# Performance work log

Measured on AMD Instinct MI355X. Metric: run time of the kernel, lower is better.

The kernel has to match this reference:

```python
import jax, jax.numpy as jnp
import numpy as np

B, N, D, H, DH, E, BIAS_DIM = 8, 512, 512, 8, 64, 32768, 8

def setup_inputs() -> dict:
    key = jax.random.key(0)
    ks = jax.random.split(key, 10)
    states = jax.random.normal(ks[0], (B, N, D), jnp.float32)
    key_states = jax.random.normal(ks[1], (B, N, D), jnp.float32)
    # causal mask, broadcastable over heads: [B,1,N,N]
    masks = jnp.broadcast_to(jnp.tril(jnp.ones((N, N), jnp.float32)), (B, 1, N, N))
    edge_type = jax.random.randint(ks[2], (E, 1), 0, BIAS_DIM, jnp.int32)
    b_idx = jax.random.randint(ks[3], (E, 1), 0, B, jnp.int32)
    q_idx = jax.random.randint(ks[4], (E, 1), 0, N, jnp.int32)
    k_idx = jax.random.randint(ks[5], (E, 1), 0, N, jnp.int32)
    attention_bias = jnp.concatenate([edge_type, b_idx, q_idx, k_idx], axis=1)
    s = 0.05
    Wq = jax.random.normal(ks[6], (D, H, DH), jnp.float32) * s
    Wk = jax.random.normal(ks[7], (D, H, DH), jnp.float32) * s
    Wv = jax.random.normal(ks[8], (D, H, DH), jnp.float32) * s
    k2 = jax.random.split(ks[9], 3)
    Wo = jax.random.normal(k2[0], (H, DH, D), jnp.float32) * s
    bias_embs = jax.random.normal(k2[1], (BIAS_DIM, DH), jnp.float32) * s
    bias_scalar = jax.random.normal(k2[2], (DH, 1), jnp.float32) * s
    return {"states": states, "key_states": key_states, "masks": masks,
            "attention_bias": attention_bias, "Wq": Wq, "Wk": Wk, "Wv": Wv,
            "Wo": Wo, "bias_embs": bias_embs, "bias_scalar": bias_scalar}

def reference(states, key_states, masks, attention_bias, Wq, Wk, Wv, Wo, bias_embs, bias_scalar):
    q = jnp.einsum('btd,dha->btha', states, Wq)
    k = jnp.einsum('btd,dha->btha', key_states, Wk)
    v = jnp.einsum('btd,dha->btha', key_states, Wv)
    alpha = jnp.einsum('bkha,bqha->bhqk', k, q)  # [B,H,Q,K]
    # sparse edge bias: embed edge types, project to scalar, scatter into [B,Q,K]
    et = attention_bias[:, 0]
    bias_vals = (bias_embs[et] @ bias_scalar)[:, 0]  # [E]
    bq, bk = alpha.shape[2], alpha.shape[3]
    bias_mat = jnp.zeros((alpha.shape[0], bq, bk), alpha.dtype)
    bias_mat = bias_mat.at[attention_bias[:, 1], attention_bias[:, 2], attention_bias[:, 3]].add(bias_vals)
    summed_keys = jnp.sum(k, axis=-1)  # [B,K,H]
    alpha = alpha + jnp.einsum('bqk,bkh->bhqk', bias_mat, summed_keys)
    alpha = alpha * jax.lax.rsqrt(jnp.float32(DH))
    neg = jnp.finfo(jnp.float32).min
    alpha = alpha * masks + (1.0 - jnp.ceil(masks)) * neg
    alpha = jax.nn.softmax(alpha, axis=-1)
    alpha = alpha * masks
    context = jnp.einsum('bhqk,bkha->bqha', alpha, v)
    return jnp.einsum('btha,had->btd', context, Wo)
```

## Files before the change

kernel.cpp:

```cpp
#include <hip/hip_runtime.h>

typedef unsigned short u16;
typedef unsigned int u32;
typedef __bf16 bf16x8 __attribute__((ext_vector_type(8)));
typedef float f32x4 __attribute__((ext_vector_type(4)));
typedef u16 u16x8 __attribute__((ext_vector_type(8)));
typedef u16 u16x4 __attribute__((ext_vector_type(4)));


__device__ __forceinline__ u16 f2b(float f) {
  union { float f; u32 i; } v; v.f = f;
  u32 r = v.i + 0x7fffu + ((v.i >> 16) & 1u);
  return (u16)(r >> 16);
}
__device__ __forceinline__ float b2f(u16 u) {
  union { u32 i; float f; } v; v.i = ((u32)u) << 16; return v.f;
}
__device__ __forceinline__ u16x8 pack8(float4 x0, float4 x1) {
  u16x8 p;
  p[0] = f2b(x0.x); p[1] = f2b(x0.y); p[2] = f2b(x0.z); p[3] = f2b(x0.w);
  p[4] = f2b(x1.x); p[5] = f2b(x1.y); p[6] = f2b(x1.z); p[7] = f2b(x1.w);
  return p;
}

__global__ __launch_bounds__(256) void prologue(
    const float* __restrict__ Wq, const float* __restrict__ Wk,
    const float* __restrict__ Wv, const float* __restrict__ Wo,
    const int* __restrict__ ab, const float* __restrict__ be,
    const float* __restrict__ bsc,
    u16* __restrict__ wbase, float* __restrict__ bias_mat, int n_edges) {
  __shared__ u16 t[32][33];
  __shared__ float tv[8];
  int bid = blockIdx.x;
  int tid = threadIdx.x;
  if (bid < 1024) {
    int z = bid >> 8, rem = bid & 255;
    int bx = rem & 15, by = rem >> 4;
    const float* src; float sc = 1.f;
    if (z == 0)      { src = Wq; sc = 0.125f; }
    else if (z == 1) { src = Wk; }
    else if (z == 2) { src = Wv; }
    else             { src = Wo; }
    u16* dst = wbase + (size_t)z * 262144;
    int tx = tid & 31, ty = tid >> 5;
    int c0 = bx * 32, r0 = by * 32;
    #pragma unroll
    for (int i = ty; i < 32; i += 8) t[i][tx] = f2b(src[(r0 + i) * 512 + c0 + tx] * sc);
    __syncthreads();
    #pragma unroll
    for (int i = ty; i < 32; i += 8) dst[(c0 + i) * 512 + r0 + tx] = t[tx][i];
  } else {
    if (tid < 8) {
      float s = 0.f;
      #pragma unroll
      for (int a = 0; a < 64; a++) s += be[tid * 64 + a] * bsc[a];
      tv[tid] = s * 0.125f;
    }
    __syncthreads();
    int e = (bid - 1024) * 256 + tid;
    if (e < n_edges) {
      int et = ab[e * 4 + 0];
      int b  = ab[e * 4 + 1];
      int qi = ab[e * 4 + 2];
      int ki = ab[e * 4 + 3];
      atomicAdd(&bias_mat[((size_t)b * 512 + qi) * 512 + ki], tv[et]);
    }
  }
}

__global__ __launch_bounds__(256) void qkv_gemm(const float* __restrict__ states,
                                                const float* __restrict__ key_states,
                                                const u16* __restrict__ wT,
                                                u16* __restrict__ qb,
                                                u16* __restrict__ kbo,
                                                u16* __restrict__ vtb,
                                                float* __restrict__ summed) {
  __shared__ u16 As[64 * 72];
  __shared__ u16 Bs[128 * 72];
  __shared__ float ssum[4][64];
  int tid = threadIdx.x;
  int lane = tid & 63, wave = tid >> 6;
  int quad = lane >> 4, ln = lane & 15;
  int row0 = blockIdx.x * 64;
  int col0 = blockIdx.y * 128;
  const float* A = (col0 < 512) ? states : key_states;
  int ara = tid >> 2, aca = (tid & 3) * 16;
  int arb = tid >> 1, acb = (tid & 1) * 32;

  f32x4 acc[4][2];
  #pragma unroll
  for (int i = 0; i < 4; i++)
    #pragma unroll
    for (int j = 0; j < 2; j++) acc[i][j] = (f32x4){0.f, 0.f, 0.f, 0.f};

  const float* ap = A + (size_t)(row0 + ara) * 512 + aca;
  const u16* bp = wT + (size_t)(col0 + arb) * 512 + acb;

  float4 fa0, fa1, fa2, fa3;
  u16x8 rb0, rb1, rb2, rb3;
  fa0 = ((const float4*)ap)[0]; fa1 = ((const float4*)ap)[1];
  fa2 = ((const float4*)ap)[2]; fa3 = ((const float4*)ap)[3];
  rb0 = *(const u16x8*)(bp + 0);  rb1 = *(const u16x8*)(bp + 8);
  rb2 = *(const u16x8*)(bp + 16); rb3 = *(const u16x8*)(bp + 24);

  for (int k0 = 0; k0 < 512; k0 += 64) {
    u16x8 pa0 = pack8(fa0, fa1);
    u16x8 pa1 = pack8(fa2, fa3);
    __syncthreads();
    *(u16x8*)&As[ara * 72 + aca + 0] = pa0;  *(u16x8*)&As[ara * 72 + aca + 8] = pa1;
    *(u16x8*)&Bs[arb * 72 + acb + 0]  = rb0;  *(u16x8*)&Bs[arb * 72 + acb + 8]  = rb1;
    *(u16x8*)&Bs[arb * 72 + acb + 16] = rb2;  *(u16x8*)&Bs[arb * 72 + acb + 24] = rb3;
    __syncthreads();
    if (k0 < 448) {
      int kn = k0 + 64;
      const float4* apn = (const float4*)(ap + kn);
      fa0 = apn[0]; fa1 = apn[1]; fa2 = apn[2]; fa3 = apn[3];
      rb0 = *(const u16x8*)(bp + kn + 0);  rb1 = *(const u16x8*)(bp + kn + 8);
      rb2 = *(const u16x8*)(bp + kn + 16); rb3 = *(const u16x8*)(bp + kn + 24);
    }
    #pragma unroll
    for (int s = 0; s < 2; s++) {
      bf16x8 af[4], bfv[2];
      #pragma unroll
      for (int i = 0; i < 4; i++)
        af[i] = *(bf16x8*)&As[(i * 16 + ln) * 72 + s * 32 + quad * 8];
      #pragma unroll
      for (int j = 0; j < 2; j++)
        bfv[j] = *(bf16x8*)&Bs[(wave * 32 + j * 16 + ln) * 72 + s * 32 + quad * 8];
      #pragma unroll
      for (int i = 0; i < 4; i++)
        #pragma unroll
        for (int j = 0; j < 2; j++)
          acc[i][j] = __builtin_amdgcn_mfma_f32_16x16x32_bf16(af[i], bfv[j], acc[i][j], 0, 0, 0);
    }
  }

  int region = col0 >> 9;
  int nbase = col0 & 511;
  if (region <= 1) {
    u16* Cout = region ? kbo : qb;
    #pragma unroll
    for (int i = 0; i < 4; i++)
      #pragma unroll
      for (int j = 0; j < 2; j++) {
        int mb = row0 + i * 16 + quad * 4;
        int n = nbase + wave * 32 + j * 16 + ln;
        #pragma unroll
        for (int r = 0; r < 4; r++)
          Cout[(size_t)(mb + r) * 512 + n] = f2b(acc[i][j][r]);
      }
    if (region == 1) {
      #pragma unroll
      for (int i = 0; i < 4; i++)
        #pragma unroll
        for (int r = 0; r < 4; r++) {
          float v = acc[i][0][r] + acc[i][1][r];
          v += __shfl_xor(v, 1);
          v += __shfl_xor(v, 2);
          v += __shfl_xor(v, 4);
          v += __shfl_xor(v, 8);
          if (ln == 0) ssum[wave][i * 16 + quad * 4 + r] = v;
        }
      __syncthreads();
      if (tid < 128) {
        int hl = tid >> 6, row = tid & 63;
        float s = ssum[hl * 2][row] + ssum[hl * 2 + 1][row];
        int m = row0 + row;
        int b = m >> 9, t = m & 511;
        int h = (nbase >> 6) + hl;
        summed[((size_t)(b * 8 + h)) * 512 + t] = s;
      }
    }
  } else {
    #pragma unroll
    for (int i = 0; i < 4; i++)
      #pragma unroll
      for (int j = 0; j < 2; j++) {
        int mb = row0 + i * 16 + quad * 4;
        int bb = mb >> 9, t0 = mb & 511;
        int a_abs = nbase + wave * 32 + j * 16 + ln;
        int h = a_abs >> 6, a = a_abs & 63;
        u16x4 p;
        p[0] = f2b(acc[i][j][0]); p[1] = f2b(acc[i][j][1]);
        p[2] = f2b(acc[i][j][2]); p[3] = f2b(acc[i][j][3]);
        *(u16x4*)&vtb[(((size_t)bb * 8 + h) * 64 + a) * 512 + t0] = p;
      }
  }
}

__global__ __launch_bounds__(256) void out_gemm(const u16* __restrict__ A,
                                                const u16* __restrict__ BT,
                                                float* __restrict__ C) {
  __shared__ u16 As[64 * 72];
  __shared__ u16 Bs[64 * 72];
  int tid = threadIdx.x;
  int lane = tid & 63, wave = tid >> 6;
  int quad = lane >> 4, ln = lane & 15;
  int wr = wave >> 1, wc = wave & 1;
  int row0 = blockIdx.x * 64;
  int col0 = blockIdx.y * 64;
  int ar = tid >> 2, ac = (tid & 3) * 16;

  f32x4 acc[2][2];
  #pragma unroll
  for (int i = 0; i < 2; i++)
    #pragma unroll
    for (int j = 0; j < 2; j++) acc[i][j] = (f32x4){0.f, 0.f, 0.f, 0.f};

  const u16* ap = A + (size_t)(row0 + ar) * 512 + ac;
  const u16* bp = BT + (size_t)(col0 + ar) * 512 + ac;

  u16x8 ra0, ra1, rb0, rb1;
  ra0 = *(const u16x8*)(ap + 0); ra1 = *(const u16x8*)(ap + 8);
  rb0 = *(const u16x8*)(bp + 0); rb1 = *(const u16x8*)(bp + 8);

  for (int k0 = 0; k0 < 512; k0 += 64) {
    __syncthreads();
    *(u16x8*)&As[ar * 72 + ac + 0] = ra0;  *(u16x8*)&As[ar * 72 + ac + 8] = ra1;
    *(u16x8*)&Bs[ar * 72 + ac + 0] = rb0;  *(u16x8*)&Bs[ar * 72 + ac + 8] = rb1;
    __syncthreads();
    if (k0 < 448) {
      int kn = k0 + 64;
      ra0 = *(const u16x8*)(ap + kn + 0); ra1 = *(const u16x8*)(ap + kn + 8);
      rb0 = *(const u16x8*)(bp + kn + 0); rb1 = *(const u16x8*)(bp + kn + 8);
    }
    #pragma unroll
    for (int s = 0; s < 2; s++) {
      bf16x8 af[2], bfv[2];
      #pragma unroll
      for (int i = 0; i < 2; i++)
        af[i] = *(bf16x8*)&As[(wr * 32 + i * 16 + ln) * 72 + s * 32 + quad * 8];
      #pragma unroll
      for (int j = 0; j < 2; j++)
        bfv[j] = *(bf16x8*)&Bs[(wc * 32 + j * 16 + ln) * 72 + s * 32 + quad * 8];
      #pragma unroll
      for (int i = 0; i < 2; i++)
        #pragma unroll
        for (int j = 0; j < 2; j++)
          acc[i][j] = __builtin_amdgcn_mfma_f32_16x16x32_bf16(af[i], bfv[j], acc[i][j], 0, 0, 0);
    }
  }
  #pragma unroll
  for (int i = 0; i < 2; i++)
    #pragma unroll
    for (int j = 0; j < 2; j++) {
      int mb = row0 + wr * 32 + i * 16 + quad * 4;
      int n = col0 + wc * 32 + j * 16 + ln;
      #pragma unroll
      for (int r = 0; r < 4; r++)
        C[(size_t)(mb + r) * 512 + n] = acc[i][j][r];
    }
}

__global__ __launch_bounds__(256) void attn_mfma(const u16* __restrict__ q,
                                                 const u16* __restrict__ k,
                                                 const u16* __restrict__ vt,
                                                 const float* __restrict__ bias_mat,
                                                 const float* __restrict__ summed,
                                                 u16* __restrict__ ctx,
                                                 float* __restrict__ Opart,
                                                 float* __restrict__ ml) {
  __shared__ u16 Qs[64 * 72];
  __shared__ u16 Ks[64 * 72];
  __shared__ u16 Vt[64 * 72];
  __shared__ u16 Ps[4][16 * 72];
  int tid = threadIdx.x;
  int wave = tid >> 6, lane = tid & 63;
  int quad = lane >> 4, ln = lane & 15;
  int p2 = blockIdx.x;
  int bh, u;
  {
    const int fours[6] = {3, 4, 6, 8, 10, 11};
    const int threes[2] = {2, 9};
    const int ones[2] = {0, 5};
    const int twos[2] = {1, 7};
    if (p2 < 384)      { bh = p2 & 63; u = fours[p2 >> 6]; }
    else if (p2 < 512) { int q2 = p2 - 384; bh = q2 & 63; u = threes[q2 >> 6]; }
    else if (p2 < 640) { int q2 = p2 - 512; bh = q2 & 63; u = ones[q2 >> 6]; }
    else               { int q2 = p2 - 640; bh = q2 & 63; u = twos[q2 >> 6]; }
  }
  int b = bh >> 3, h = bh & 7;
  int qt, kb0, kbe, part = 0;
  bool partial;
  if (u < 4) { qt = u; kb0 = 0; kbe = u; partial = false; }
  else {
    int v = u - 4; qt = 4 + (v >> 1); part = v & 1; partial = true;
    if (part == 0) { kb0 = 0; kbe = 3; } else { kb0 = 4; kbe = qt; }
  }
  int q0 = qt * 64;

  int sr = tid >> 2;
  int sc2 = (tid & 3) * 16;

  {
    const u16* qp = q + ((size_t)(b * 512 + q0 + sr)) * 512 + h * 64 + sc2;
    *(u16x8*)&Qs[sr * 72 + sc2] = *(const u16x8*)qp;
    *(u16x8*)&Qs[sr * 72 + sc2 + 8] = *(const u16x8*)(qp + 8);
  }

  float m_r[4], l_r[4];
  f32x4 o[4];
  #pragma unroll
  for (int r = 0; r < 4; r++) { m_r[r] = -3.40282347e38f; l_r[r] = 0.f; }
  #pragma unroll
  for (int nt = 0; nt < 4; nt++) o[nt] = (f32x4){0.f, 0.f, 0.f, 0.f};

  const u16* kp0 = k + ((size_t)(b * 512 + sr)) * 512 + h * 64 + sc2;
  const u16* vp0 = vt + ((size_t)(bh * 64 + sr)) * 512 + sc2;

  u16x8 rk0 = *(const u16x8*)(kp0 + (size_t)kb0 * 64 * 512);
  u16x8 rk1 = *(const u16x8*)(kp0 + (size_t)kb0 * 64 * 512 + 8);
  u16x8 rv0 = *(const u16x8*)(vp0 + kb0 * 64);
  u16x8 rv1 = *(const u16x8*)(vp0 + kb0 * 64 + 8);

  int qrow = q0 + wave * 16 + quad * 4;

  float c_skv[4], c_bias[4][4];
  #pragma unroll
  for (int nt = 0; nt < 4; nt++) {
    int t = kb0 * 64 + nt * 16 + ln;
    c_skv[nt] = summed[bh * 512 + t];
    const float* bp2 = bias_mat + ((size_t)(b * 512 + qrow)) * 512 + t;
    #pragma unroll
    for (int r = 0; r < 4; r++) c_bias[nt][r] = bp2[(size_t)r * 512];
  }

  for (int kb = kb0; kb <= kbe; kb++) {
    __syncthreads();
    *(u16x8*)&Ks[sr * 72 + sc2] = rk0;
    *(u16x8*)&Ks[sr * 72 + sc2 + 8] = rk1;
    *(u16x8*)&Vt[sr * 72 + sc2] = rv0;
    *(u16x8*)&Vt[sr * 72 + sc2 + 8] = rv1;
    __syncthreads();

    float n_skv[4], n_bias[4][4];
    if (kb < kbe) {
      const u16* kp = kp0 + (size_t)(kb + 1) * 64 * 512;
      const u16* vp = vp0 + (kb + 1) * 64;
      rk0 = *(const u16x8*)kp;
      rk1 = *(const u16x8*)(kp + 8);
      rv0 = *(const u16x8*)vp;
      rv1 = *(const u16x8*)(vp + 8);
      #pragma unroll
      for (int nt = 0; nt < 4; nt++) {
        int t = (kb + 1) * 64 + nt * 16 + ln;
        n_skv[nt] = summed[bh * 512 + t];
        const float* bp2 = bias_mat + ((size_t)(b * 512 + qrow)) * 512 + t;
        #pragma unroll
        for (int r = 0; r < 4; r++) n_bias[nt][r] = bp2[(size_t)r * 512];
      }
    }

    bf16x8 aq0 = *(bf16x8*)&Qs[(wave * 16 + ln) * 72 + quad * 8];
    bf16x8 aq1 = *(bf16x8*)&Qs[(wave * 16 + ln) * 72 + 32 + quad * 8];
    f32x4 s[4];
    #pragma unroll
    for (int nt = 0; nt < 4; nt++) {
      bf16x8 b0 = *(bf16x8*)&Ks[(nt * 16 + ln) * 72 + quad * 8];
      bf16x8 b1 = *(bf16x8*)&Ks[(nt * 16 + ln) * 72 + 32 + quad * 8];
      s[nt] = (f32x4){0.f, 0.f, 0.f, 0.f};
      s[nt] = __builtin_amdgcn_mfma_f32_16x16x32_bf16(aq0, b0, s[nt], 0, 0, 0);
      s[nt] = __builtin_amdgcn_mfma_f32_16x16x32_bf16(aq1, b1, s[nt], 0, 0, 0);
    }

    #pragma unroll
    for (int nt = 0; nt < 4; nt++) {
      int t = kb * 64 + nt * 16 + ln;
      #pragma unroll
      for (int r = 0; r < 4; r++) {
        float val = s[nt][r] + c_bias[nt][r] * c_skv[nt];
        s[nt][r] = (t <= qrow + r) ? val : -3.40282347e38f;
      }
    }

    float alpha[4];
    #pragma unroll
    for (int r = 0; r < 4; r++) {
      float tm = fmaxf(fmaxf(s[0][r], s[1][r]), fmaxf(s[2][r], s[3][r]));
      #pragma unroll
      for (int off = 8; off; off >>= 1) tm = fmaxf(tm, __shfl_xor(tm, off));
      float mn = fmaxf(m_r[r], tm);
      alpha[r] = __expf(m_r[r] - mn);
      m_r[r] = mn;
      float rs = 0.f;
      #pragma unroll
      for (int nt = 0; nt < 4; nt++) {
        float pp = __expf(s[nt][r] - mn);
        s[nt][r] = pp;
        rs += pp;
      }
      #pragma unroll
      for (int off = 8; off; off >>= 1) rs += __shfl_xor(rs, off);
      l_r[r] = l_r[r] * alpha[r] + rs;
    }

    #pragma unroll
    for (int nt = 0; nt < 4; nt++)
      #pragma unroll
      for (int r = 0; r < 4; r++)
        Ps[wave][(quad * 4 + r) * 72 + nt * 16 + ln] = f2b(s[nt][r]);
    #pragma unroll
    for (int nt = 0; nt < 4; nt++)
      #pragma unroll
      for (int r = 0; r < 4; r++)
        o[nt][r] *= alpha[r];

    bf16x8 ap0 = *(bf16x8*)&Ps[wave][ln * 72 + quad * 8];
    bf16x8 ap1 = *(bf16x8*)&Ps[wave][ln * 72 + 32 + quad * 8];
    #pragma unroll
    for (int nt = 0; nt < 4; nt++) {
      bf16x8 b0 = *(bf16x8*)&Vt[(nt * 16 + ln) * 72 + quad * 8];
      bf16x8 b1 = *(bf16x8*)&Vt[(nt * 16 + ln) * 72 + 32 + quad * 8];
      o[nt] = __builtin_amdgcn_mfma_f32_16x16x32_bf16(ap0, b0, o[nt], 0, 0, 0);
      o[nt] = __builtin_amdgcn_mfma_f32_16x16x32_bf16(ap1, b1, o[nt], 0, 0, 0);
    }

    if (kb < kbe) {
      #pragma unroll
      for (int nt = 0; nt < 4; nt++) {
        c_skv[nt] = n_skv[nt];
        #pragma unroll
        for (int r = 0; r < 4; r++) c_bias[nt][r] = n_bias[nt][r];
      }
    }
  }

  if (!partial) {
    #pragma unroll
    for (int r = 0; r < 4; r++) {
      float inv = 1.f / l_r[r];
      int qr2 = qrow + r;
      u16* dst = ctx + ((size_t)(b * 512 + qr2)) * 512 + h * 64;
      #pragma unroll
      for (int nt = 0; nt < 4; nt++)
        dst[nt * 16 + ln] = f2b(o[nt][r] * inv);
    }
  } else {
    #pragma unroll
    for (int r = 0; r < 4; r++) {
      int row = qrow + r - 256;
      float* dst = Opart + (((size_t)(part * 64 + bh)) * 256 + row) * 64;
      #pragma unroll
      for (int nt = 0; nt < 4; nt++)
        dst[nt * 16 + ln] = o[nt][r];
    }
    if (ln == 0) {
      #pragma unroll
      for (int r = 0; r < 4; r++) {
        int row = qrow + r - 256;
        float* mp = ml + (((size_t)(part * 64 + bh)) * 256 + row) * 2;
        mp[0] = m_r[r];
        mp[1] = l_r[r];
      }
    }
  }
}

__global__ __launch_bounds__(256) void attn_merge(const float* __restrict__ Opart,
                                                  const float* __restrict__ ml,
                                                  u16* __restrict__ ctx) {
  int gid = blockIdx.x * 256 + threadIdx.x;
  int col = gid & 63;
  int row = (gid >> 6) & 255;
  int bh = gid >> 14;
  size_t i0 = (size_t)bh * 256 + row;
  size_t i1 = (size_t)(64 + bh) * 256 + row;
  float m0 = ml[i0 * 2], l0 = ml[i0 * 2 + 1];
  float m1 = ml[i1 * 2], l1 = ml[i1 * 2 + 1];
  float m = fmaxf(m0, m1);
  float a0 = __expf(m0 - m), a1 = __expf(m1 - m);
  float l = l0 * a0 + l1 * a1;
  float O0 = Opart[i0 * 64 + col], O1 = Opart[i1 * 64 + col];
  float val = (O0 * a0 + O1 * a1) / l;
  int b = bh >> 3, h = bh & 7, qrow = 256 + row;
  ctx[((size_t)(b * 512 + qrow)) * 512 + h * 64 + col] = f2b(val);
}

extern "C" void kernel_launch(void* const* d_in, const int* in_sizes, int n_in,
                              void* d_out, int out_size, void* d_ws, size_t ws_size,
                              hipStream_t stream) {
  const float* states     = (const float*)d_in[0];
  const float* key_states = (const float*)d_in[1];
  const int*   ab         = (const int*)d_in[3];
  const float* Wq         = (const float*)d_in[4];
  const float* Wk         = (const float*)d_in[5];
  const float* Wv         = (const float*)d_in[6];
  const float* Wo         = (const float*)d_in[7];
  const float* be         = (const float*)d_in[8];
  const float* bsc        = (const float*)d_in[9];
  float* out = (float*)d_out;

  char* ws = (char*)d_ws;
  const size_t MB = 1024 * 1024;
  u16* wbase    = (u16*)(ws);
  u16* wot      = (u16*)(ws + 1536 * 1024);
  u16* qb       = (u16*)(ws + 2 * MB);
  u16* kbo      = (u16*)(ws + 6 * MB);
  u16* vtb      = (u16*)(ws + 10 * MB);
  u16* ctxb     = (u16*)(ws + 14 * MB);
  float* bias_m = (float*)(ws + 18 * MB);
  float* summed = (float*)(ws + 26 * MB);
  float* Opart  = (float*)(ws + 27 * MB);
  float* mlbuf  = (float*)(ws + 35 * MB);

  int n_edges = in_sizes[3] / 4;

  hipMemsetAsync(bias_m, 0, (size_t)8 * MB, stream);
  prologue<<<dim3(1024 + (n_edges + 255) / 256), 256, 0, stream>>>(
      Wq, Wk, Wv, Wo, ab, be, bsc, wbase, bias_m, n_edges);
  qkv_gemm<<<dim3(64, 12), 256, 0, stream>>>(states, key_states, wbase, qb, kbo, vtb, summed);
  attn_mfma<<<dim3(768), 256, 0, stream>>>(qb, kbo, vtb, bias_m, summed, ctxb, Opart, mlbuf);
  attn_merge<<<dim3(4096), 256, 0, stream>>>(Opart, mlbuf, ctxb);
  out_gemm<<<dim3(64, 8), 256, 0, stream>>>(ctxb, wot, out);
}
```

Measured before the change: 135.4 us.

## Fuse split-KV merge into output GEMM and fold memset and scatter into existing kernels

Removes the hipMemset and the separate attn_merge launch. The prologue now zeroes the bias matrix alongside the weight transposes. The edge-bias atomic scatter moves into extra blocks of the QKV GEMM launch, and the output GEMM combines the two partial attention outputs on the fly for the second half of query rows. This cuts two launches and a round trip of the merged context through global memory. In exchange, the out_gemm A-tile load path for merged rows reads twice the fp32 data and does exp and normalization work per tile.

```diff
diff --git a/kernel.cpp b/kernel.cpp
--- a/kernel.cpp
+++ b/kernel.cpp
@@ -13,9 +13,6 @@
   u32 r = v.i + 0x7fffu + ((v.i >> 16) & 1u);
   return (u16)(r >> 16);
 }
-__device__ __forceinline__ float b2f(u16 u) {
-  union { u32 i; float f; } v; v.i = ((u32)u) << 16; return v.f;
-}
 __device__ __forceinline__ u16x8 pack8(float4 x0, float4 x1) {
   u16x8 p;
   p[0] = f2b(x0.x); p[1] = f2b(x0.y); p[2] = f2b(x0.z); p[3] = f2b(x0.w);
@@ -26,11 +23,8 @@
 __global__ __launch_bounds__(256) void prologue(
     const float* __restrict__ Wq, const float* __restrict__ Wk,
     const float* __restrict__ Wv, const float* __restrict__ Wo,
-    const int* __restrict__ ab, const float* __restrict__ be,
-    const float* __restrict__ bsc,
-    u16* __restrict__ wbase, float* __restrict__ bias_mat, int n_edges) {
+    u16* __restrict__ wbase, float* __restrict__ bias_mat) {
   __shared__ u16 t[32][33];
-  __shared__ float tv[8];
   int bid = blockIdx.x;
   int tid = threadIdx.x;
   if (bid < 1024) {
@@ -50,6 +44,33 @@
     #pragma unroll
     for (int i = ty; i < 32; i += 8) dst[(c0 + i) * 512 + r0 + tx] = t[tx][i];
   } else {
+    int gid = (bid - 1024) * 256 + tid;
+    float4 z4 = (float4){0.f, 0.f, 0.f, 0.f};
+    float4* dst = (float4*)bias_mat + (size_t)gid * 4;
+    dst[0] = z4; dst[1] = z4; dst[2] = z4; dst[3] = z4;
+  }
+}
+
+__global__ __launch_bounds__(256) void qkv_gemm(const float* __restrict__ states,
+                                                const float* __restrict__ key_states,
+                                                const u16* __restrict__ wT,
+                                                u16* __restrict__ qb,
+                                                u16* __restrict__ kbo,
+                                                u16* __restrict__ vtb,
+                                                float* __restrict__ summed,
+                                                const int* __restrict__ ab,
+                                                const float* __restrict__ be,
+                                                const float* __restrict__ bsc,
+                                                float* __restrict__ bias_mat,
+                                                int n_edges) {
+  __shared__ u16 As[64 * 72];
+  __shared__ u16 Bs[128 * 72];
+  __shared__ float ssum[4][64];
+  __shared__ float tv[8];
+  int bid = blockIdx.x;
+  int tid = threadIdx.x;
+
+  if (bid >= 768) {
     if (tid < 8) {
       float s = 0.f;
       #pragma unroll
@@ -57,7 +78,7 @@
       tv[tid] = s * 0.125f;
     }
     __syncthreads();
-    int e = (bid - 1024) * 256 + tid;
+    int e = (bid - 768) * 256 + tid;
     if (e < n_edges) {
       int et = ab[e * 4 + 0];
       int b  = ab[e * 4 + 1];
@@ -65,24 +86,14 @@
       int ki = ab[e * 4 + 3];
       atomicAdd(&bias_mat[((size_t)b * 512 + qi) * 512 + ki], tv[et]);
     }
-  }
-}
-
-__global__ __launch_bounds__(256) void qkv_gemm(const float* __restrict__ states,
-                                                const float* __restrict__ key_states,
-                                                const u16* __restrict__ wT,
-                                                u16* __restrict__ qb,
-                                                u16* __restrict__ kbo,
-                                                u16* __restrict__ vtb,
-                                                float* __restrict__ summed) {
-  __shared__ u16 As[64 * 72];
-  __shared__ u16 Bs[128 * 72];
-  __shared__ float ssum[4][64];
-  int tid = threadIdx.x;
+    return;
+  }
+
   int lane = tid & 63, wave = tid >> 6;
   int quad = lane >> 4, ln = lane & 15;
-  int row0 = blockIdx.x * 64;
-  int col0 = blockIdx.y * 128;
+  int bx = bid & 63, by = bid >> 6;
+  int row0 = bx * 64;
+  int col0 = by * 128;
   const float* A = (col0 < 512) ? states : key_states;
   int ara = tid >> 2, aca = (tid & 3) * 16;
   int arb = tid >> 1, acb = (tid & 1) * 32;
@@ -186,70 +197,6 @@
         *(u16x4*)&vtb[(((size_t)bb * 8 + h) * 64 + a) * 512 + t0] = p;
       }
   }
-}
-
-__global__ __launch_bounds__(256) void out_gemm(const u16* __restrict__ A,
-                                                const u16* __restrict__ BT,
-                                                float* __restrict__ C) {
-  __shared__ u16 As[64 * 72];
-  __shared__ u16 Bs[64 * 72];
-  int tid = threadIdx.x;
-  int lane = tid & 63, wave = tid >> 6;
-  int quad = lane >> 4, ln = lane & 15;
-  int wr = wave >> 1, wc = wave & 1;
-  int row0 = blockIdx.x * 64;
-  int col0 = blockIdx.y * 64;
-  int ar = tid >> 2, ac = (tid & 3) * 16;
-
-  f32x4 acc[2][2];
-  #pragma unroll
-  for (int i = 0; i < 2; i++)
-    #pragma unroll
-    for (int j = 0; j < 2; j++) acc[i][j] = (f32x4){0.f, 0.f, 0.f, 0.f};
-
-  const u16* ap = A + (size_t)(row0 + ar) * 512 + ac;
-  const u16* bp = BT + (size_t)(col0 + ar) * 512 + ac;
-
-  u16x8 ra0, ra1, rb0, rb1;
-  ra0 = *(const u16x8*)(ap + 0); ra1 = *(const u16x8*)(ap + 8);
-  rb0 = *(const u16x8*)(bp + 0); rb1 = *(const u16x8*)(bp + 8);
-
-  for (int k0 = 0; k0 < 512; k0 += 64) {
-    __syncthreads();
-    *(u16x8*)&As[ar * 72 + ac + 0] = ra0;  *(u16x8*)&As[ar * 72 + ac + 8] = ra1;
-    *(u16x8*)&Bs[ar * 72 + ac + 0] = rb0;  *(u16x8*)&Bs[ar * 72 + ac + 8] = rb1;
-    __syncthreads();
-    if (k0 < 448) {
-      int kn = k0 + 64;
-      ra0 = *(const u16x8*)(ap + kn + 0); ra1 = *(const u16x8*)(ap + kn + 8);
-      rb0 = *(const u16x8*)(bp + kn + 0); rb1 = *(const u16x8*)(bp + kn + 8);
-    }
-    #pragma unroll
-    for (int s = 0; s < 2; s++) {
-      bf16x8 af[2], bfv[2];
-      #pragma unroll
-      for (int i = 0; i < 2; i++)
-        af[i] = *(bf16x8*)&As[(wr * 32 + i * 16 + ln) * 72 + s * 32 + quad * 8];
-      #pragma unroll
-      for (int j = 0; j < 2; j++)
-        bfv[j] = *(bf16x8*)&Bs[(wc * 32 + j * 16 + ln) * 72 + s * 32 + quad * 8];
-      #pragma unroll
-      for (int i = 0; i < 2; i++)
-        #pragma unroll
-        for (int j = 0; j < 2; j++)
-          acc[i][j] = __builtin_amdgcn_mfma_f32_16x16x32_bf16(af[i], bfv[j], acc[i][j], 0, 0, 0);
-    }
-  }
-  #pragma unroll
-  for (int i = 0; i < 2; i++)
-    #pragma unroll
-    for (int j = 0; j < 2; j++) {
-      int mb = row0 + wr * 32 + i * 16 + quad * 4;
-      int n = col0 + wc * 32 + j * 16 + ln;
-      #pragma unroll
-      for (int r = 0; r < 4; r++)
-        C[(size_t)(mb + r) * 512 + n] = acc[i][j][r];
-    }
 }
 
 __global__ __launch_bounds__(256) void attn_mfma(const u16* __restrict__ q,
@@ -456,24 +403,116 @@
   }
 }
 
-__global__ __launch_bounds__(256) void attn_merge(const float* __restrict__ Opart,
-                                                  const float* __restrict__ ml,
-                                                  u16* __restrict__ ctx) {
-  int gid = blockIdx.x * 256 + threadIdx.x;
-  int col = gid & 63;
-  int row = (gid >> 6) & 255;
-  int bh = gid >> 14;
-  size_t i0 = (size_t)bh * 256 + row;
-  size_t i1 = (size_t)(64 + bh) * 256 + row;
-  float m0 = ml[i0 * 2], l0 = ml[i0 * 2 + 1];
-  float m1 = ml[i1 * 2], l1 = ml[i1 * 2 + 1];
-  float m = fmaxf(m0, m1);
-  float a0 = __expf(m0 - m), a1 = __expf(m1 - m);
-  float l = l0 * a0 + l1 * a1;
-  float O0 = Opart[i0 * 64 + col], O1 = Opart[i1 * 64 + col];
-  float val = (O0 * a0 + O1 * a1) / l;
-  int b = bh >> 3, h = bh & 7, qrow = 256 + row;
-  ctx[((size_t)(b * 512 + qrow)) * 512 + h * 64 + col] = f2b(val);
+__global__ __launch_bounds__(256) void out_gemm(const u16* __restrict__ A,
+                                                const u16* __restrict__ BT,
+                                                const float* __restrict__ Opart,
+                                                const float* __restrict__ ml,
+                                                float* __restrict__ C) {
+  __shared__ u16 As[64 * 72];
+  __shared__ u16 Bs[64 * 72];
+  int tid = threadIdx.x;
+  int lane = tid & 63, wave = tid >> 6;
+  int quad = lane >> 4, ln = lane & 15;
+  int wr = wave >> 1, wc = wave & 1;
+  int row0 = blockIdx.x * 64;
+  int col0 = blockIdx.y * 64;
+  int ar = tid >> 2, ac = (tid & 3) * 16;
+  bool merged = (row0 & 256) != 0;
+  int mrow = row0 + ar;
+  int bb = mrow >> 9;
+  int rrow = (mrow & 511) - 256;
+
+  f32x4 acc[2][2];
+  #pragma unroll
+  for (int i = 0; i < 2; i++)
+    #pragma unroll
+    for (int j = 0; j < 2; j++) acc[i][j] = (f32x4){0.f, 0.f, 0.f, 0.f};
+
+  const u16* ap = A + (size_t)mrow * 512 + ac;
+  const u16* bp = BT + (size_t)(col0 + ar) * 512 + ac;
+
+  u16x8 ra0, ra1, rb0, rb1;
+  float4 g0, g1, g2, g3, hh0, hh1, hh2, hh3;
+  float cm0, cl0, cm1, cl1;
+  if (!merged) {
+    ra0 = *(const u16x8*)(ap + 0); ra1 = *(const u16x8*)(ap + 8);
+  } else {
+    size_t i0 = (size_t)(bb * 8 + 0) * 256 + rrow;
+    size_t i1 = (size_t)(64 + bb * 8 + 0) * 256 + rrow;
+    const float4* O0 = (const float4*)(Opart + i0 * 64 + ac);
+    const float4* O1 = (const float4*)(Opart + i1 * 64 + ac);
+    g0 = O0[0]; g1 = O0[1]; g2 = O0[2]; g3 = O0[3];
+    hh0 = O1[0]; hh1 = O1[1]; hh2 = O1[2]; hh3 = O1[3];
+    cm0 = ml[i0 * 2]; cl0 = ml[i0 * 2 + 1];
+    cm1 = ml[i1 * 2]; cl1 = ml[i1 * 2 + 1];
+  }
+  rb0 = *(const u16x8*)(bp + 0); rb1 = *(const u16x8*)(bp + 8);
+
+  for (int k0 = 0; k0 < 512; k0 += 64) {
+    u16x8 pa0, pa1;
+    if (!merged) {
+      pa0 = ra0; pa1 = ra1;
+    } else {
+      float mm = fmaxf(cm0, cm1);
+      float e0 = __expf(cm0 - mm), e1 = __expf(cm1 - mm);
+      float inv = 1.f / (cl0 * e0 + cl1 * e1);
+      e0 *= inv; e1 *= inv;
+      pa0[0] = f2b(g0.x * e0 + hh0.x * e1); pa0[1] = f2b(g0.y * e0 + hh0.y * e1);
+      pa0[2] = f2b(g0.z * e0 + hh0.z * e1); pa0[3] = f2b(g0.w * e0 + hh0.w * e1);
+      pa0[4] = f2b(g1.x * e0 + hh1.x * e1); pa0[5] = f2b(g1.y * e0 + hh1.y * e1);
+      pa0[6] = f2b(g1.z * e0 + hh1.z * e1); pa0[7] = f2b(g1.w * e0 + hh1.w * e1);
+      pa1[0] = f2b(g2.x * e0 + hh2.x * e1); pa1[1] = f2b(g2.y * e0 + hh2.y * e1);
+      pa1[2] = f2b(g2.z * e0 + hh2.z * e1); pa1[3] = f2b(g2.w * e0 + hh2.w * e1);
+      pa1[4] = f2b(g3.x * e0 + hh3.x * e1); pa1[5] = f2b(g3.y * e0 + hh3.y * e1);
+      pa1[6] = f2b(g3.z * e0 + hh3.z * e1); pa1[7] = f2b(g3.w * e0 + hh3.w * e1);
+    }
+    __syncthreads();
+    *(u16x8*)&As[ar * 72 + ac + 0] = pa0;  *(u16x8*)&As[ar * 72 + ac + 8] = pa1;
+    *(u16x8*)&Bs[ar * 72 + ac + 0] = rb0;  *(u16x8*)&Bs[ar * 72 + ac + 8] = rb1;
+    __syncthreads();
+    if (k0 < 448) {
+      int kn = k0 + 64;
+      if (!merged) {
+        ra0 = *(const u16x8*)(ap + kn + 0); ra1 = *(const u16x8*)(ap + kn + 8);
+      } else {
+        int h = kn >> 6;
+        size_t i0 = (size_t)(bb * 8 + h) * 256 + rrow;
+        size_t i1 = (size_t)(64 + bb * 8 + h) * 256 + rrow;
+        const float4* O0 = (const float4*)(Opart + i0 * 64 + ac);
+        const float4* O1 = (const float4*)(Opart + i1 * 64 + ac);
+        g0 = O0[0]; g1 = O0[1]; g2 = O0[2]; g3 = O0[3];
+        hh0 = O1[0]; hh1 = O1[1]; hh2 = O1[2]; hh3 = O1[3];
+        cm0 = ml[i0 * 2]; cl0 = ml[i0 * 2 + 1];
+        cm1 = ml[i1 * 2]; cl1 = ml[i1 * 2 + 1];
+      }
+      rb0 = *(const u16x8*)(bp + kn + 0); rb1 = *(const u16x8*)(bp + kn + 8);
+    }
+    #pragma unroll
+    for (int s = 0; s < 2; s++) {
+      bf16x8 af[2], bfv[2];
+      #pragma unroll
+      for (int i = 0; i < 2; i++)
+        af[i] = *(bf16x8*)&As[(wr * 32 + i * 16 + ln) * 72 + s * 32 + quad * 8];
+      #pragma unroll
+      for (int j = 0; j < 2; j++)
+        bfv[j] = *(bf16x8*)&Bs[(wc * 32 + j * 16 + ln) * 72 + s * 32 + quad * 8];
+      #pragma unroll
+      for (int i = 0; i < 2; i++)
+        #pragma unroll
+        for (int j = 0; j < 2; j++)
+          acc[i][j] = __builtin_amdgcn_mfma_f32_16x16x32_bf16(af[i], bfv[j], acc[i][j], 0, 0, 0);
+    }
+  }
+  #pragma unroll
+  for (int i = 0; i < 2; i++)
+    #pragma unroll
+    for (int j = 0; j < 2; j++) {
+      int mb = row0 + wr * 32 + i * 16 + quad * 4;
+      int n = col0 + wc * 32 + j * 16 + ln;
+      #pragma unroll
+      for (int r = 0; r < 4; r++)
+        C[(size_t)(mb + r) * 512 + n] = acc[i][j][r];
+    }
 }
 
 extern "C" void kernel_launch(void* const* d_in, const int* in_sizes, int n_in,
@@ -505,11 +544,9 @@
 
   int n_edges = in_sizes[3] / 4;
 
-  hipMemsetAsync(bias_m, 0, (size_t)8 * MB, stream);
-  prologue<<<dim3(1024 + (n_edges + 255) / 256), 256, 0, stream>>>(
-      Wq, Wk, Wv, Wo, ab, be, bsc, wbase, bias_m, n_edges);
-  qkv_gemm<<<dim3(64, 12), 256, 0, stream>>>(states, key_states, wbase, qb, kbo, vtb, summed);
+  prologue<<<dim3(1536), 256, 0, stream>>>(Wq, Wk, Wv, Wo, wbase, bias_m);
+  qkv_gemm<<<dim3(768 + (n_edges + 255) / 256), 256, 0, stream>>>(
+      states, key_states, wbase, qb, kbo, vtb, summed, ab, be, bsc, bias_m, n_edges);
   attn_mfma<<<dim3(768), 256, 0, stream>>>(qb, kbo, vtb, bias_m, summed, ctxb, Opart, mlbuf);
-  attn_merge<<<dim3(4096), 256, 0, stream>>>(Opart, mlbuf, ctxb);
-  out_gemm<<<dim3(64, 8), 256, 0, stream>>>(ctxb, wot, out);
-}
+  out_gemm<<<dim3(64, 8), 256, 0, stream>>>(ctxb, wot, Opart, mlbuf, out);
+}
```

New measurement: 134.7 us. No clear change (-0.5%).

## Restructure attention into per-wave 16-row tiles and fold bias zeroing and scatter into other kernels

Applied to the files above, without the earlier changes.

Attention is rewritten so each wave handles one 16-row query tile. Rows are paired (j, 31-j, j+8, 23-j) so every block does a balanced amount of causal work, which removes the split-K partial path and the merge kernel. K and V fragments are loaded straight from global memory into registers, with no shared-memory staging and no block barriers. The bias matrix is now zeroed inside the prologue instead of by a memset, and the edge scatter moves into extra blocks of the QKV GEMM launch, cutting the kernel count. The trade-off is that waves no longer share K/V loads through LDS, so each wave re-reads them from global memory or cache.

```diff
diff --git a/kernel.cpp b/kernel.cpp
--- a/kernel.cpp
+++ b/kernel.cpp
@@ -13,9 +13,6 @@
   u32 r = v.i + 0x7fffu + ((v.i >> 16) & 1u);
   return (u16)(r >> 16);
 }
-__device__ __forceinline__ float b2f(u16 u) {
-  union { u32 i; float f; } v; v.i = ((u32)u) << 16; return v.f;
-}
 __device__ __forceinline__ u16x8 pack8(float4 x0, float4 x1) {
   u16x8 p;
   p[0] = f2b(x0.x); p[1] = f2b(x0.y); p[2] = f2b(x0.z); p[3] = f2b(x0.w);
@@ -26,11 +23,8 @@
 __global__ __launch_bounds__(256) void prologue(
     const float* __restrict__ Wq, const float* __restrict__ Wk,
     const float* __restrict__ Wv, const float* __restrict__ Wo,
-    const int* __restrict__ ab, const float* __restrict__ be,
-    const float* __restrict__ bsc,
-    u16* __restrict__ wbase, float* __restrict__ bias_mat, int n_edges) {
+    u16* __restrict__ wbase, float* __restrict__ bias_mat) {
   __shared__ u16 t[32][33];
-  __shared__ float tv[8];
   int bid = blockIdx.x;
   int tid = threadIdx.x;
   if (bid < 1024) {
@@ -50,6 +44,33 @@
     #pragma unroll
     for (int i = ty; i < 32; i += 8) dst[(c0 + i) * 512 + r0 + tx] = t[tx][i];
   } else {
+    int gid = (bid - 1024) * 256 + tid;
+    float4 z4 = (float4){0.f, 0.f, 0.f, 0.f};
+    float4* dst = (float4*)bias_mat + (size_t)gid * 4;
+    dst[0] = z4; dst[1] = z4; dst[2] = z4; dst[3] = z4;
+  }
+}
+
+__global__ __launch_bounds__(256) void qkv_gemm(const float* __restrict__ states,
+                                                const float* __restrict__ key_states,
+                                                const u16* __restrict__ wT,
+                                                u16* __restrict__ qb,
+                                                u16* __restrict__ kbo,
+                                                u16* __restrict__ vtb,
+                                                float* __restrict__ summed,
+                                                const int* __restrict__ ab,
+                                                const float* __restrict__ be,
+                                                const float* __restrict__ bsc,
+                                                float* __restrict__ bias_mat,
+                                                int n_edges) {
+  __shared__ u16 As[64 * 72];
+  __shared__ u16 Bs[128 * 72];
+  __shared__ float ssum[4][64];
+  __shared__ float tv[8];
+  int bid = blockIdx.x;
+  int tid = threadIdx.x;
+
+  if (bid >= 768) {
     if (tid < 8) {
       float s = 0.f;
       #pragma unroll
@@ -57,7 +78,7 @@
       tv[tid] = s * 0.125f;
     }
     __syncthreads();
-    int e = (bid - 1024) * 256 + tid;
+    int e = (bid - 768) * 256 + tid;
     if (e < n_edges) {
       int et = ab[e * 4 + 0];
       int b  = ab[e * 4 + 1];
@@ -65,24 +86,14 @@
       int ki = ab[e * 4 + 3];
       atomicAdd(&bias_mat[((size_t)b * 512 + qi) * 512 + ki], tv[et]);
     }
-  }
-}
-
-__global__ __launch_bounds__(256) void qkv_gemm(const float* __restrict__ states,
-                                                const float* __restrict__ key_states,
-                                                const u16* __restrict__ wT,
-                                                u16* __restrict__ qb,
-                                                u16* __restrict__ kbo,
-                                                u16* __restrict__ vtb,
-                                                float* __restrict__ summed) {
-  __shared__ u16 As[64 * 72];
-  __shared__ u16 Bs[128 * 72];
-  __shared__ float ssum[4][64];
-  int tid = threadIdx.x;
+    return;
+  }
+
   int lane = tid & 63, wave = tid >> 6;
   int quad = lane >> 4, ln = lane & 15;
-  int row0 = blockIdx.x * 64;
-  int col0 = blockIdx.y * 128;
+  int bx = bid & 63, by = bid >> 6;
+  int row0 = bx * 64;
+  int col0 = by * 128;
   const float* A = (col0 < 512) ? states : key_states;
   int ara = tid >> 2, aca = (tid & 3) * 16;
   int arb = tid >> 1, acb = (tid & 1) * 32;
@@ -188,6 +199,146 @@
   }
 }
 
+__global__ __launch_bounds__(256) void attn_mfma(const u16* __restrict__ q,
+                                                 const u16* __restrict__ k,
+                                                 const u16* __restrict__ vt,
+                                                 const float* __restrict__ bias_mat,
+                                                 const float* __restrict__ summed,
+                                                 u16* __restrict__ ctx) {
+  __shared__ u16 Ps[4][16 * 72];
+  int tid = threadIdx.x;
+  int wave = tid >> 6, lane = tid & 63;
+  int quad = lane >> 4, ln = lane & 15;
+  int blk = blockIdx.x;
+  int bh = blk >> 3, j = blk & 7;
+  int b = bh >> 3, h = bh & 7;
+  int r;
+  if (wave == 0)      r = j;
+  else if (wave == 1) r = 31 - j;
+  else if (wave == 2) r = j + 8;
+  else                r = 23 - j;
+  int q0 = r * 16;
+  int kbe = r >> 2;
+  int qrow = q0 + quad * 4;
+
+  const u16* qp = q + ((size_t)(b * 512 + q0 + ln)) * 512 + h * 64 + quad * 8;
+  bf16x8 aq0 = *(const bf16x8*)qp;
+  bf16x8 aq1 = *(const bf16x8*)(qp + 32);
+
+  float m_r[4], l_r[4];
+  f32x4 o[4];
+  #pragma unroll
+  for (int rr = 0; rr < 4; rr++) { m_r[rr] = -3.40282347e38f; l_r[rr] = 0.f; }
+  #pragma unroll
+  for (int nt = 0; nt < 4; nt++) o[nt] = (f32x4){0.f, 0.f, 0.f, 0.f};
+
+  const u16* kp = k + ((size_t)(b * 512 + ln)) * 512 + h * 64 + quad * 8;
+  const u16* vp = vt + ((size_t)(bh * 64 + ln)) * 512 + quad * 8;
+
+  for (int kb = 0; kb <= kbe; kb++) {
+    bf16x8 kf[4][2];
+    #pragma unroll
+    for (int nt = 0; nt < 4; nt++) {
+      const u16* kpp = kp + (size_t)(kb * 64 + nt * 16) * 512;
+      kf[nt][0] = *(const bf16x8*)kpp;
+      kf[nt][1] = *(const bf16x8*)(kpp + 32);
+    }
+    float skv[4], bias_r[4][4];
+    #pragma unroll
+    for (int nt = 0; nt < 4; nt++) {
+      int t = kb * 64 + nt * 16 + ln;
+      skv[nt] = summed[bh * 512 + t];
+      const float* bp2 = bias_mat + ((size_t)(b * 512 + qrow)) * 512 + t;
+      #pragma unroll
+      for (int rr = 0; rr < 4; rr++) bias_r[nt][rr] = bp2[(size_t)rr * 512];
+    }
+
+    f32x4 s[4];
+    #pragma unroll
+    for (int nt = 0; nt < 4; nt++) {
+      s[nt] = (f32x4){0.f, 0.f, 0.f, 0.f};
+      s[nt] = __builtin_amdgcn_mfma_f32_16x16x32_bf16(aq0, kf[nt][0], s[nt], 0, 0, 0);
+      s[nt] = __builtin_amdgcn_mfma_f32_16x16x32_bf16(aq1, kf[nt][1], s[nt], 0, 0, 0);
+    }
+
+    bf16x8 vf[4][2];
+    #pragma unroll
+    for (int nt2 = 0; nt2 < 4; nt2++) {
+      const u16* vpp = vp + (size_t)(nt2 * 16) * 512 + kb * 64;
+      vf[nt2][0] = *(const bf16x8*)vpp;
+      vf[nt2][1] = *(const bf16x8*)(vpp + 32);
+    }
+
+    if (kb == kbe) {
+      #pragma unroll
+      for (int nt = 0; nt < 4; nt++) {
+        int t = kb * 64 + nt * 16 + ln;
+        #pragma unroll
+        for (int rr = 0; rr < 4; rr++) {
+          float val = s[nt][rr] + bias_r[nt][rr] * skv[nt];
+          s[nt][rr] = (t <= qrow + rr) ? val : -3.40282347e38f;
+        }
+      }
+    } else {
+      #pragma unroll
+      for (int nt = 0; nt < 4; nt++)
+        #pragma unroll
+        for (int rr = 0; rr < 4; rr++)
+          s[nt][rr] += bias_r[nt][rr] * skv[nt];
+    }
+
+    float alpha[4];
+    #pragma unroll
+    for (int rr = 0; rr < 4; rr++) {
+      float tm = fmaxf(fmaxf(s[0][rr], s[1][rr]), fmaxf(s[2][rr], s[3][rr]));
+      #pragma unroll
+      for (int off = 8; off; off >>= 1) tm = fmaxf(tm, __shfl_xor(tm, off));
+      float mn = fmaxf(m_r[rr], tm);
+      alpha[rr] = __expf(m_r[rr] - mn);
+      m_r[rr] = mn;
+      float rs = 0.f;
+      #pragma unroll
+      for (int nt = 0; nt < 4; nt++) {
+        float pp = __expf(s[nt][rr] - mn);
+        s[nt][rr] = pp;
+        rs += pp;
+      }
+      #pragma unroll
+      for (int off = 8; off; off >>= 1) rs += __shfl_xor(rs, off);
+      l_r[rr] = l_r[rr] * alpha[rr] + rs;
+    }
+
+    #pragma unroll
+    for (int nt = 0; nt < 4; nt++)
+      #pragma unroll
+      for (int rr = 0; rr < 4; rr++)
+        Ps[wave][(quad * 4 + rr) * 72 + nt * 16 + ln] = f2b(s[nt][rr]);
+    #pragma unroll
+    for (int nt = 0; nt < 4; nt++)
+      #pragma unroll
+      for (int rr = 0; rr < 4; rr++)
+        o[nt][rr] *= alpha[rr];
+
+    bf16x8 ap0 = *(bf16x8*)&Ps[wave][ln * 72 + quad * 8];
+    bf16x8 ap1 = *(bf16x8*)&Ps[wave][ln * 72 + 32 + quad * 8];
+    #pragma unroll
+    for (int nt2 = 0; nt2 < 4; nt2++) {
+      o[nt2] = __builtin_amdgcn_mfma_f32_16x16x32_bf16(ap0, vf[nt2][0], o[nt2], 0, 0, 0);
+      o[nt2] = __builtin_amdgcn_mfma_f32_16x16x32_bf16(ap1, vf[nt2][1], o[nt2], 0, 0, 0);
+    }
+  }
+
+  #pragma unroll
+  for (int rr = 0; rr < 4; rr++) {
+    float inv = 1.f / l_r[rr];
+    int qr2 = qrow + rr;
+    u16* dst = ctx + ((size_t)(b * 512 + qr2)) * 512 + h * 64;
+    #pragma unroll
+    for (int nt = 0; nt < 4; nt++)
+      dst[nt * 16 + ln] = f2b(o[nt][rr] * inv);
+  }
+}
+
 __global__ __launch_bounds__(256) void out_gemm(const u16* __restrict__ A,
                                                 const u16* __restrict__ BT,
                                                 float* __restrict__ C) {
@@ -250,230 +401,6 @@
       for (int r = 0; r < 4; r++)
         C[(size_t)(mb + r) * 512 + n] = acc[i][j][r];
     }
-}
-
-__global__ __launch_bounds__(256) void attn_mfma(const u16* __restrict__ q,
-                                                 const u16* __restrict__ k,
-                                                 const u16* __restrict__ vt,
-                                                 const float* __restrict__ bias_mat,
-                                                 const float* __restrict__ summed,
-                                                 u16* __restrict__ ctx,
-                                                 float* __restrict__ Opart,
-                                                 float* __restrict__ ml) {
-  __shared__ u16 Qs[64 * 72];
-  __shared__ u16 Ks[64 * 72];
-  __shared__ u16 Vt[64 * 72];
-  __shared__ u16 Ps[4][16 * 72];
-  int tid = threadIdx.x;
-  int wave = tid >> 6, lane = tid & 63;
-  int quad = lane >> 4, ln = lane & 15;
-  int p2 = blockIdx.x;
-  int bh, u;
-  {
-    const int fours[6] = {3, 4, 6, 8, 10, 11};
-    const int threes[2] = {2, 9};
-    const int ones[2] = {0, 5};
-    const int twos[2] = {1, 7};
-    if (p2 < 384)      { bh = p2 & 63; u = fours[p2 >> 6]; }
-    else if (p2 < 512) { int q2 = p2 - 384; bh = q2 & 63; u = threes[q2 >> 6]; }
-    else if (p2 < 640) { int q2 = p2 - 512; bh = q2 & 63; u = ones[q2 >> 6]; }
-    else               { int q2 = p2 - 640; bh = q2 & 63; u = twos[q2 >> 6]; }
-  }
-  int b = bh >> 3, h = bh & 7;
-  int qt, kb0, kbe, part = 0;
-  bool partial;
-  if (u < 4) { qt = u; kb0 = 0; kbe = u; partial = false; }
-  else {
-    int v = u - 4; qt = 4 + (v >> 1); part = v & 1; partial = true;
-    if (part == 0) { kb0 = 0; kbe = 3; } else { kb0 = 4; kbe = qt; }
-  }
-  int q0 = qt * 64;
-
-  int sr = tid >> 2;
-  int sc2 = (tid & 3) * 16;
-
-  {
-    const u16* qp = q + ((size_t)(b * 512 + q0 + sr)) * 512 + h * 64 + sc2;
-    *(u16x8*)&Qs[sr * 72 + sc2] = *(const u16x8*)qp;
-    *(u16x8*)&Qs[sr * 72 + sc2 + 8] = *(const u16x8*)(qp + 8);
-  }
-
-  float m_r[4], l_r[4];
-  f32x4 o[4];
-  #pragma unroll
-  for (int r = 0; r < 4; r++) { m_r[r] = -3.40282347e38f; l_r[r] = 0.f; }
-  #pragma unroll
-  for (int nt = 0; nt < 4; nt++) o[nt] = (f32x4){0.f, 0.f, 0.f, 0.f};
-
-  const u16* kp0 = k + ((size_t)(b * 512 + sr)) * 512 + h * 64 + sc2;
-  const u16* vp0 = vt + ((size_t)(bh * 64 + sr)) * 512 + sc2;
-
-  u16x8 rk0 = *(const u16x8*)(kp0 + (size_t)kb0 * 64 * 512);
-  u16x8 rk1 = *(const u16x8*)(kp0 + (size_t)kb0 * 64 * 512 + 8);
-  u16x8 rv0 = *(const u16x8*)(vp0 + kb0 * 64);
-  u16x8 rv1 = *(const u16x8*)(vp0 + kb0 * 64 + 8);
-
-  int qrow = q0 + wave * 16 + quad * 4;
-
-  float c_skv[4], c_bias[4][4];
-  #pragma unroll
-  for (int nt = 0; nt < 4; nt++) {
-    int t = kb0 * 64 + nt * 16 + ln;
-    c_skv[nt] = summed[bh * 512 + t];
-    const float* bp2 = bias_mat + ((size_t)(b * 512 + qrow)) * 512 + t;
-    #pragma unroll
-    for (int r = 0; r < 4; r++) c_bias[nt][r] = bp2[(size_t)r * 512];
-  }
-
-  for (int kb = kb0; kb <= kbe; kb++) {
-    __syncthreads();
-    *(u16x8*)&Ks[sr * 72 + sc2] = rk0;
-    *(u16x8*)&Ks[sr * 72 + sc2 + 8] = rk1;
-    *(u16x8*)&Vt[sr * 72 + sc2] = rv0;
-    *(u16x8*)&Vt[sr * 72 + sc2 + 8] = rv1;
-    __syncthreads();
-
-    float n_skv[4], n_bias[4][4];
-    if (kb < kbe) {
-      const u16* kp = kp0 + (size_t)(kb + 1) * 64 * 512;
-      const u16* vp = vp0 + (kb + 1) * 64;
-      rk0 = *(const u16x8*)kp;
-      rk1 = *(const u16x8*)(kp + 8);
-      rv0 = *(const u16x8*)vp;
-      rv1 = *(const u16x8*)(vp + 8);
-      #pragma unroll
-      for (int nt = 0; nt < 4; nt++) {
-        int t = (kb + 1) * 64 + nt * 16 + ln;
-        n_skv[nt] = summed[bh * 512 + t];
-        const float* bp2 = bias_mat + ((size_t)(b * 512 + qrow)) * 512 + t;
-        #pragma unroll
-        for (int r = 0; r < 4; r++) n_bias[nt][r] = bp2[(size_t)r * 512];
-      }
-    }
-
-    bf16x8 aq0 = *(bf16x8*)&Qs[(wave * 16 + ln) * 72 + quad * 8];
-    bf16x8 aq1 = *(bf16x8*)&Qs[(wave * 16 + ln) * 72 + 32 + quad * 8];
-    f32x4 s[4];
-    #pragma unroll
-    for (int nt = 0; nt < 4; nt++) {
-      bf16x8 b0 = *(bf16x8*)&Ks[(nt * 16 + ln) * 72 + quad * 8];
-      bf16x8 b1 = *(bf16x8*)&Ks[(nt * 16 + ln) * 72 + 32 + quad * 8];
-      s[nt] = (f32x4){0.f, 0.f, 0.f, 0.f};
-      s[nt] = __builtin_amdgcn_mfma_f32_16x16x32_bf16(aq0, b0, s[nt], 0, 0, 0);
-      s[nt] = __builtin_amdgcn_mfma_f32_16x16x32_bf16(aq1, b1, s[nt], 0, 0, 0);
-    }
-
-    #pragma unroll
-    for (int nt = 0; nt < 4; nt++) {
-      int t = kb * 64 + nt * 16 + ln;
-      #pragma unroll
-      for (int r = 0; r < 4; r++) {
-        float val = s[nt][r] + c_bias[nt][r] * c_skv[nt];
-        s[nt][r] = (t <= qrow + r) ? val : -3.40282347e38f;
-      }
-    }
-
-    float alpha[4];
-    #pragma unroll
-    for (int r = 0; r < 4; r++) {
-      float tm = fmaxf(fmaxf(s[0][r], s[1][r]), fmaxf(s[2][r], s[3][r]));
-      #pragma unroll
-      for (int off = 8; off; off >>= 1) tm = fmaxf(tm, __shfl_xor(tm, off));
-      float mn = fmaxf(m_r[r], tm);
-      alpha[r] = __expf(m_r[r] - mn);
-      m_r[r] = mn;
-      float rs = 0.f;
-      #pragma unroll
-      for (int nt = 0; nt < 4; nt++) {
-        float pp = __expf(s[nt][r] - mn);
-        s[nt][r] = pp;
-        rs += pp;
-      }
-      #pragma unroll
-      for (int off = 8; off; off >>= 1) rs += __shfl_xor(rs, off);
-      l_r[r] = l_r[r] * alpha[r] + rs;
-    }
-
-    #pragma unroll
-    for (int nt = 0; nt < 4; nt++)
-      #pragma unroll
-      for (int r = 0; r < 4; r++)
-        Ps[wave][(quad * 4 + r) * 72 + nt * 16 + ln] = f2b(s[nt][r]);
-    #pragma unroll
-    for (int nt = 0; nt < 4; nt++)
-      #pragma unroll
-      for (int r = 0; r < 4; r++)
-        o[nt][r] *= alpha[r];
-
-    bf16x8 ap0 = *(bf16x8*)&Ps[wave][ln * 72 + quad * 8];
-    bf16x8 ap1 = *(bf16x8*)&Ps[wave][ln * 72 + 32 + quad * 8];
-    #pragma unroll
-    for (int nt = 0; nt < 4; nt++) {
-      bf16x8 b0 = *(bf16x8*)&Vt[(nt * 16 + ln) * 72 + quad * 8];
-      bf16x8 b1 = *(bf16x8*)&Vt[(nt * 16 + ln) * 72 + 32 + quad * 8];
-      o[nt] = __builtin_amdgcn_mfma_f32_16x16x32_bf16(ap0, b0, o[nt], 0, 0, 0);
-      o[nt] = __builtin_amdgcn_mfma_f32_16x16x32_bf16(ap1, b1, o[nt], 0, 0, 0);
-    }
-
-    if (kb < kbe) {
-      #pragma unroll
-      for (int nt = 0; nt < 4; nt++) {
-        c_skv[nt] = n_skv[nt];
-        #pragma unroll
-        for (int r = 0; r < 4; r++) c_bias[nt][r] = n_bias[nt][r];
-      }
-    }
-  }
-
-  if (!partial) {
-    #pragma unroll
-    for (int r = 0; r < 4; r++) {
-      float inv = 1.f / l_r[r];
-      int qr2 = qrow + r;
-      u16* dst = ctx + ((size_t)(b * 512 + qr2)) * 512 + h * 64;
-      #pragma unroll
-      for (int nt = 0; nt < 4; nt++)
-        dst[nt * 16 + ln] = f2b(o[nt][r] * inv);
-    }
-  } else {
-    #pragma unroll
-    for (int r = 0; r < 4; r++) {
-      int row = qrow + r - 256;
-      float* dst = Opart + (((size_t)(part * 64 + bh)) * 256 + row) * 64;
-      #pragma unroll
-      for (int nt = 0; nt < 4; nt++)
-        dst[nt * 16 + ln] = o[nt][r];
-    }
-    if (ln == 0) {
-      #pragma unroll
-      for (int r = 0; r < 4; r++) {
-        int row = qrow + r - 256;
-        float* mp = ml + (((size_t)(part * 64 + bh)) * 256 + row) * 2;
-        mp[0] = m_r[r];
-        mp[1] = l_r[r];
-      }
-    }
-  }
-}
-
-__global__ __launch_bounds__(256) void attn_merge(const float* __restrict__ Opart,
-                                                  const float* __restrict__ ml,
-                                                  u16* __restrict__ ctx) {
-  int gid = blockIdx.x * 256 + threadIdx.x;
-  int col = gid & 63;
-  int row = (gid >> 6) & 255;
-  int bh = gid >> 14;
-  size_t i0 = (size_t)bh * 256 + row;
-  size_t i1 = (size_t)(64 + bh) * 256 + row;
-  float m0 = ml[i0 * 2], l0 = ml[i0 * 2 + 1];
-  float m1 = ml[i1 * 2], l1 = ml[i1 * 2 + 1];
-  float m = fmaxf(m0, m1);
-  float a0 = __expf(m0 - m), a1 = __expf(m1 - m);
-  float l = l0 * a0 + l1 * a1;
-  float O0 = Opart[i0 * 64 + col], O1 = Opart[i1 * 64 + col];
-  float val = (O0 * a0 + O1 * a1) / l;
-  int b = bh >> 3, h = bh & 7, qrow = 256 + row;
-  ctx[((size_t)(b * 512 + qrow)) * 512 + h * 64 + col] = f2b(val);
 }
 
 extern "C" void kernel_launch(void* const* d_in, const int* in_sizes, int n_in,
@@ -500,16 +427,12 @@
   u16* ctxb     = (u16*)(ws + 14 * MB);
   float* bias_m = (float*)(ws + 18 * MB);
   float* summed = (float*)(ws + 26 * MB);
-  float* Opart  = (float*)(ws + 27 * MB);
-  float* mlbuf  = (float*)(ws + 35 * MB);
 
   int n_edges = in_sizes[3] / 4;
 
-  hipMemsetAsync(bias_m, 0, (size_t)8 * MB, stream);
-  prologue<<<dim3(1024 + (n_edges + 255) / 256), 256, 0, stream>>>(
-      Wq, Wk, Wv, Wo, ab, be, bsc, wbase, bias_m, n_edges);
-  qkv_gemm<<<dim3(64, 12), 256, 0, stream>>>(states, key_states, wbase, qb, kbo, vtb, summed);
-  attn_mfma<<<dim3(768), 256, 0, stream>>>(qb, kbo, vtb, bias_m, summed, ctxb, Opart, mlbuf);
-  attn_merge<<<dim3(4096), 256, 0, stream>>>(Opart, mlbuf, ctxb);
+  prologue<<<dim3(1536), 256, 0, stream>>>(Wq, Wk, Wv, Wo, wbase, bias_m);
+  qkv_gemm<<<dim3(768 + (n_edges + 255) / 256), 256, 0, stream>>>(
+      states, key_states, wbase, qb, kbo, vtb, summed, ab, be, bsc, bias_m, n_edges);
+  attn_mfma<<<dim3(512), 256, 0, stream>>>(qb, kbo, vtb, bias_m, summed, ctxb);
   out_gemm<<<dim3(64, 8), 256, 0, stream>>>(ctxb, wot, out);
 }
```

Result: no change. 136.0 us (+0.4%).
